# Performance work log

Hardware: AMD Instinct MI355X
Metric: run time of the kernel (lower is better)

Reference implementation:

```python
import jax, jax.numpy as jnp
import numpy as np

NEG_SLOPE = 0.2   # PyG GATConv default negative_slope
LN_EPS = 1e-5
SOFTMAX_EPS = 1e-16  # PyG softmax denominator eps


def setup_inputs() -> dict:
    key = jax.random.key(0)
    ks = jax.random.split(key, 6)
    N, IN, OUT, H, E = 100000, 128, 64, 2, 1600000
    X = jax.random.normal(ks[0], (N, IN), dtype=jnp.float32)
    edge_index = jax.random.randint(ks[1], (2, E), 0, N, dtype=jnp.int64)
    W = jax.random.normal(ks[2], (H * OUT, IN), dtype=jnp.float32) * 0.05
    att_src = jax.random.normal(ks[3], (H, OUT), dtype=jnp.float32) * 0.05
    att_dst = jax.random.normal(ks[4], (H, OUT), dtype=jnp.float32) * 0.05
    bias = jnp.zeros((OUT,), dtype=jnp.float32)
    ln_gamma = jnp.ones((OUT,), dtype=jnp.float32)
    ln_beta = jnp.zeros((OUT,), dtype=jnp.float32)
    return {"X": X, "edge_index": edge_index, "W": W, "att_src": att_src,
            "att_dst": att_dst, "bias": bias, "ln_gamma": ln_gamma, "ln_beta": ln_beta}


def reference(X, edge_index, W, att_src, att_dst, bias, ln_gamma, ln_beta):
    N = X.shape[0]
    H, F = att_src.shape
    # PyG GATConv default: add self-loops
    loops = jnp.arange(N, dtype=edge_index.dtype)
    src = jnp.concatenate([edge_index[0], loops])  # [Et]
    dst = jnp.concatenate([edge_index[1], loops])  # [Et]
    # linear projection: x' = X @ W^T  -> [N, H, F]
    x = (X @ W.T).reshape(N, H, F)
    # per-node attention logits  [N, H]
    a_src = jnp.einsum('nhf,hf->nh', x, att_src)
    a_dst = jnp.einsum('nhf,hf->nh', x, att_dst)
    # per-edge logits, leaky relu  [Et, H]
    e = jax.nn.leaky_relu(a_src[src] + a_dst[dst], NEG_SLOPE)
    # segment softmax over incoming edges of each dst node
    m = jax.ops.segment_max(e, dst, num_segments=N)          # [N, H]
    ex = jnp.exp(e - m[dst])
    denom = jax.ops.segment_sum(ex, dst, num_segments=N)     # [N, H]
    alpha = ex / (denom[dst] + SOFTMAX_EPS)                  # [Et, H]
    # weighted scatter-add of source features
    msg = x[src] * alpha[:, :, None]                         # [Et, H, F]
    out = jax.ops.segment_sum(msg, dst, num_segments=N)      # [N, H, F]
    # concat=False -> mean over heads, then bias
    out = out.mean(axis=1) + bias                            # [N, F]
    # LayerNorm over features
    mu = out.mean(axis=-1, keepdims=True)
    var = ((out - mu) ** 2).mean(axis=-1, keepdims=True)
    h = (out - mu) * jax.lax.rsqrt(var + LN_EPS) * ln_gamma + ln_beta
    return h
```

## Files before the change

kernel.cpp:

```cpp
#include <hip/hip_runtime.h>
#include <hip/hip_bf16.h>

#define NEG_SLOPE 0.2f
#define LN_EPS 1e-5f
#define SM_EPS 1e-16f

typedef __attribute__((ext_vector_type(8))) short bf16x8;
typedef __attribute__((ext_vector_type(4))) float f32x4;

__device__ inline unsigned short f2bf(float f) {
    unsigned u = __float_as_uint(f);
    return (unsigned short)((u + 0x7FFFu + ((u >> 16) & 1u)) >> 16);
}
__device__ inline float bf_lo(unsigned int v) { return __uint_as_float(v << 16); }
__device__ inline float bf_hi(unsigned int v) { return __uint_as_float(v & 0xffff0000u); }
__device__ inline float rdlane(float v, int l) {
    return __uint_as_float(__builtin_amdgcn_readlane(__float_as_uint(v), l));
}

#define NBIN 512
#define BCAP 4864
#define SCHUNK 4096
#define CURPAD 16

__global__ __launch_bounds__(256) void k_gemm(const float* __restrict__ X,
                                              const float* __restrict__ W,
                                              const float* __restrict__ att_src,
                                              const float* __restrict__ att_dst,
                                              unsigned int* __restrict__ xp,
                                              float2* __restrict__ aS,
                                              float2* __restrict__ aD,
                                              int* __restrict__ binCursor, int N) {
    __shared__ unsigned short Ws[128 * 136];
    __shared__ unsigned short Xs[64 * 136];
    const int t = threadIdx.x;
    const int b0 = blockIdx.x * 64;
    const int lane = t & 63;
    const int w = t >> 6;
    const int c15 = lane & 15;
    const int quad = lane >> 4;

    if (blockIdx.x == 0) {
        for (int i = t; i < NBIN; i += 256) binCursor[i * CURPAD] = i * BCAP;
    }

#pragma unroll
    for (int i = 0; i < 16; ++i) {
        int f = i * 256 + t;
        int nr = f >> 5;
        int q = f & 31;
        float4 v = reinterpret_cast<const float4*>(W)[nr * 32 + q];
        ushort4 b;
        b.x = f2bf(v.x); b.y = f2bf(v.y); b.z = f2bf(v.z); b.w = f2bf(v.w);
        *reinterpret_cast<ushort4*>(&Ws[nr * 136 + q * 4]) = b;
    }
#pragma unroll
    for (int i = 0; i < 8; ++i) {
        int f = i * 256 + t;
        int m = f >> 5;
        int q = f & 31;
        int gr = b0 + m;
        if (gr >= N) gr = N - 1;
        float4 v = reinterpret_cast<const float4*>(X)[(size_t)gr * 32 + q];
        ushort4 b;
        b.x = f2bf(v.x); b.y = f2bf(v.y); b.z = f2bf(v.z); b.w = f2bf(v.w);
        *reinterpret_cast<ushort4*>(&Xs[m * 136 + q * 4]) = b;
    }
    __syncthreads();

    f32x4 acc[8];
#pragma unroll
    for (int ct = 0; ct < 8; ++ct) acc[ct] = (f32x4){0.f, 0.f, 0.f, 0.f};

#pragma unroll
    for (int kc = 0; kc < 4; ++kc) {
        bf16x8 af = *reinterpret_cast<const bf16x8*>(
            &Xs[(w * 16 + c15) * 136 + kc * 32 + quad * 8]);
#pragma unroll
        for (int ct = 0; ct < 8; ++ct) {
            bf16x8 bfr = *reinterpret_cast<const bf16x8*>(
                &Ws[(ct * 16 + c15) * 136 + kc * 32 + quad * 8]);
            acc[ct] = __builtin_amdgcn_mfma_f32_16x16x32_bf16(af, bfr, acc[ct], 0, 0, 0);
        }
    }

    float attS[8], attD[8];
#pragma unroll
    for (int ct = 0; ct < 8; ++ct) {
        attS[ct] = att_src[ct * 16 + c15];
        attD[ct] = att_dst[ct * 16 + c15];
    }

#pragma unroll
    for (int r = 0; r < 4; ++r) {
        int row = b0 + w * 16 + quad * 4 + r;
        float s0 = 0.f, s1 = 0.f, d0 = 0.f, d1 = 0.f;
#pragma unroll
        for (int ct = 0; ct < 4; ++ct) {
            s0 += acc[ct][r] * attS[ct];
            d0 += acc[ct][r] * attD[ct];
            s1 += acc[ct + 4][r] * attS[ct + 4];
            d1 += acc[ct + 4][r] * attD[ct + 4];
        }
#pragma unroll
        for (int o = 1; o < 16; o <<= 1) {
            s0 += __shfl_xor(s0, o);
            s1 += __shfl_xor(s1, o);
            d0 += __shfl_xor(d0, o);
            d1 += __shfl_xor(d1, o);
        }
        if (row < N) {
#pragma unroll
            for (int ct = 0; ct < 4; ++ct) {
                unsigned int p = (unsigned int)f2bf(acc[ct][r]) |
                                 ((unsigned int)f2bf(acc[ct + 4][r]) << 16);
                xp[(size_t)row * 64 + ct * 16 + c15] = p;
            }
            if (c15 == 0) {
                aS[row] = make_float2(s0, s1);
                aD[row] = make_float2(d0, d1);
            }
        }
    }
}

__global__ __launch_bounds__(256) void k_scatter(const int* __restrict__ ei,
                                                 int* __restrict__ binCursor,
                                                 unsigned int* __restrict__ tmp,
                                                 int E) {
    __shared__ int off[NBIN];
    const int t = threadIdx.x;
    const int base = blockIdx.x * SCHUNK;

    int bn[16];
    unsigned int pe[16];
#pragma unroll
    for (int k = 0; k < 16; ++k) {
        int i = base + k * 256 + t;
        if (i < E) {
            int s = ei[i];
            int d = ei[E + i];
            bn[k] = d >> 8;
            pe[k] = ((unsigned)(d & 255) << 24) | (unsigned)s;
        } else {
            bn[k] = -1;
        }
    }

    for (int i = t; i < NBIN; i += 256) off[i] = 0;
    __syncthreads();
#pragma unroll
    for (int k = 0; k < 16; ++k)
        if (bn[k] >= 0) atomicAdd(&off[bn[k]], 1);
    __syncthreads();
    for (int i = t; i < NBIN; i += 256) {
        int h = off[i];
        off[i] = h ? atomicAdd(&binCursor[i * CURPAD], h) : 0;
    }
    __syncthreads();
#pragma unroll
    for (int k = 0; k < 16; ++k) {
        if (bn[k] >= 0) {
            int p = atomicAdd(&off[bn[k]], 1);
            tmp[p] = pe[k];
        }
    }
}

__global__ __launch_bounds__(512) void k_bucket(const unsigned int* __restrict__ tmp,
                                                const int* __restrict__ binCursor,
                                                unsigned int* __restrict__ csr,
                                                unsigned int* __restrict__ rowPtr,
                                                int N) {
    __shared__ int cnt[256];
    __shared__ int cur[256];
    __shared__ int lds[4];
    const int t = threadIdx.x;
    const int b = blockIdx.x;
    const int start = b * BCAP;
    int m = binCursor[b * CURPAD] - start;
    if (m > BCAP) m = BCAP;

    if (t < 256) cnt[t] = 0;
    __syncthreads();

    for (int k = t; k < m; k += 512) {
        atomicAdd(&cnt[tmp[start + k] >> 24], 1);
    }
    __syncthreads();

    const int lane = t & 63, w = t >> 6;
    int v = 0, incl = 0;
    if (t < 256) {
        v = cnt[t];
        incl = v;
#pragma unroll
        for (int o = 1; o < 64; o <<= 1) {
            int u = __shfl_up(incl, o);
            if (lane >= o) incl += u;
        }
        if (lane == 63) lds[w] = incl;
    }
    __syncthreads();
    if (t == 0) {
        int run = 0;
        for (int i = 0; i < 4; ++i) { int tv = lds[i]; lds[i] = run; run += tv; }
    }
    __syncthreads();
    if (t < 256) {
        int excl = lds[w] + incl - v;
        cur[t] = excl;
        int d = b * 256 + t;
        if (d < N) rowPtr[d] = (unsigned)(start + excl) | ((unsigned)v << 22);
    }
    __syncthreads();

    for (int k = t; k < m; k += 512) {
        unsigned int e = tmp[start + k];
        int p = atomicAdd(&cur[e >> 24], 1);
        csr[start + p] = e & 0x00FFFFFFu;
    }
}

__global__ __launch_bounds__(256) void k_agg(const unsigned int* __restrict__ xp,
                                             const float2* __restrict__ aS,
                                             const float2* __restrict__ aD,
                                             const unsigned int* __restrict__ rowPtr,
                                             const unsigned int* __restrict__ csr,
                                             const float* __restrict__ bias,
                                             const float* __restrict__ gamma,
                                             const float* __restrict__ beta,
                                             float* __restrict__ out, int N) {
    const int w = threadIdx.x >> 6, lane = threadIdx.x & 63;
    const int n = blockIdx.x * 4 + w;
    if (n >= N) return;

    const float* aSf = (const float*)aS;

    float2 a = aS[n];
    float2 ad2 = aD[n];
    float f0 = a.x + ad2.x; f0 = fmaxf(f0, NEG_SLOPE * f0);
    float f1 = a.y + ad2.y; f1 = fmaxf(f1, NEG_SLOPE * f1);
    float us0 = __expf(f0), us1 = __expf(f1);

    unsigned int vself = xp[((unsigned)n << 6) | lane];
    float S0 = us0 * bf_lo(vself);
    float S1 = us1 * bf_hi(vself);
    float D0 = us0, D1 = us1;

    unsigned int pr = rowPtr[n];
    const int jb = (int)(pr & 0x3FFFFFu);
    const int deg = (int)(pr >> 22);
    const int je = jb + deg;
    const int nb = (deg + 7) >> 3;

    const int eq = lane & 7;
    const int hsel = (lane >> 3) & 1;
    const float adv = hsel ? ad2.y : ad2.x;

    float Dacc = 0.f;
    int j = jb;
    unsigned int cc[8];
    unsigned int myc = 0;

    if (nb > 0) {
        int ju = __builtin_amdgcn_readfirstlane(jb);
        int last = __builtin_amdgcn_readfirstlane(je - 1);
#pragma unroll
        for (int q = 0; q < 8; ++q) {
            int idx = ju + q; if (idx > last) idx = last;
            cc[q] = csr[idx];
        }
        int mi = ju + eq; if (mi > last) mi = last;
        myc = csr[mi];
    }

    for (int bI = 0; bI < nb; ++bI) {
        const int limit = je - j;
        float av = aSf[(myc << 1) | (unsigned)hsel];
        unsigned int v[8];
#pragma unroll
        for (int q = 0; q < 8; ++q)
            v[q] = (xp + ((size_t)cc[q] << 6))[lane];
        unsigned int cn[8], mn;
        {
            int jn = (bI + 1 < nb) ? (j + 8) : jb;
            int ju = __builtin_amdgcn_readfirstlane(jn);
            int last = __builtin_amdgcn_readfirstlane(je - 1);
#pragma unroll
            for (int q = 0; q < 8; ++q) {
                int idx = ju + q; if (idx > last) idx = last;
                cn[q] = csr[idx];
            }
            int mi = ju + eq; if (mi > last) mi = last;
            mn = csr[mi];
        }
        float g = av + adv; g = fmaxf(g, NEG_SLOPE * g);
        float u = (eq < limit) ? __expf(g) : 0.f;
        Dacc += u;
#pragma unroll
        for (int q = 0; q < 8; ++q) {
            float u0 = rdlane(u, q);
            float u1 = rdlane(u, q + 8);
            S0 = fmaf(u0, bf_lo(v[q]), S0);
            S1 = fmaf(u1, bf_hi(v[q]), S1);
        }
#pragma unroll
        for (int q = 0; q < 8; ++q) cc[q] = cn[q];
        myc = mn;
        j += 8;
    }

    Dacc += __shfl_xor(Dacc, 1);
    Dacc += __shfl_xor(Dacc, 2);
    Dacc += __shfl_xor(Dacc, 4);
    D0 += rdlane(Dacc, 0);
    D1 += rdlane(Dacc, 8);

    float o = (0.5f / (D0 + SM_EPS)) * S0 + (0.5f / (D1 + SM_EPS)) * S1 + bias[lane];

    float mu = o;
#pragma unroll
    for (int d = 32; d > 0; d >>= 1) mu += __shfl_xor(mu, d);
    mu *= (1.0f / 64.0f);
    float dv = o - mu;
    float var = dv * dv;
#pragma unroll
    for (int d = 32; d > 0; d >>= 1) var += __shfl_xor(var, d);
    var *= (1.0f / 64.0f);
    out[(size_t)n * 64 + lane] = dv * rsqrtf(var + LN_EPS) * gamma[lane] + beta[lane];
}

extern "C" void kernel_launch(void* const* d_in, const int* in_sizes, int n_in,
                              void* d_out, int out_size, void* d_ws, size_t ws_size,
                              hipStream_t stream) {
    const float* X        = (const float*)d_in[0];
    const int*   ei       = (const int*)d_in[1];
    const float* W        = (const float*)d_in[2];
    const float* att_src  = (const float*)d_in[3];
    const float* att_dst  = (const float*)d_in[4];
    const float* bias     = (const float*)d_in[5];
    const float* ln_gamma = (const float*)d_in[6];
    const float* ln_beta  = (const float*)d_in[7];
    float* out = (float*)d_out;

    const int N = in_sizes[0] / 128;
    const int E = in_sizes[1] / 2;
    const int NBUCK = (N + 255) / 256;

    char* ws = (char*)d_ws;
    size_t off = 0;
    auto alloc = [&](size_t bytes) {
        size_t o = off;
        off += (bytes + 255) & ~(size_t)255;
        return o;
    };
    unsigned int* xp     = (unsigned int*)(ws + alloc((size_t)N * 64 * 4));
    float2* aS           = (float2*)(ws + alloc((size_t)N * 8));
    float2* aD           = (float2*)(ws + alloc((size_t)N * 8));
    unsigned int* rowPtr = (unsigned int*)(ws + alloc((size_t)N * 4));
    unsigned int* csr    = (unsigned int*)(ws + alloc((size_t)NBIN * BCAP * 4));
    unsigned int* tmp    = (unsigned int*)(ws + alloc((size_t)NBIN * BCAP * 4));
    int* binCursor       = (int*)(ws + alloc(NBIN * CURPAD * 4));

    k_gemm<<<(N + 63) / 64, 256, 0, stream>>>(X, W, att_src, att_dst, xp, aS, aD,
                                              binCursor, N);
    k_scatter<<<(E + SCHUNK - 1) / SCHUNK, 256, 0, stream>>>(ei, binCursor, tmp, E);
    k_bucket<<<NBUCK, 512, 0, stream>>>(tmp, binCursor, csr, rowPtr, N);
    k_agg<<<(N + 3) / 4, 256, 0, stream>>>(xp, aS, aD, rowPtr, csr,
                                           bias, ln_gamma, ln_beta, out, N);
}
```

Measured before the change: 221.5 us.

## Merge GEMM and edge scatter into one kernel to overlap independent work

Fuses the projection GEMM and the edge-binning scatter into a single launch, where the first SB blocks do the scatter and the rest do the GEMM, so the two independent stages can run at the same time on the GPU. The bin cursors become relative counts that start at zero, reset with a memset, and the bin base offset is added at use. This saves a kernel launch and lets the memory-bound scatter overlap with the compute-bound GEMM. The cost is an extra memset call and a shared-memory footprint sized for the larger GEMM branch, which may limit occupancy for the scatter blocks.

Measured after the change: 215.0 us. 3.0% less time.

```diff
diff --git a/kernel.cpp b/kernel.cpp
--- a/kernel.cpp
+++ b/kernel.cpp
@@ -23,26 +23,67 @@
 #define SCHUNK 4096
 #define CURPAD 16
 
-__global__ __launch_bounds__(256) void k_gemm(const float* __restrict__ X,
-                                              const float* __restrict__ W,
-                                              const float* __restrict__ att_src,
-                                              const float* __restrict__ att_dst,
-                                              unsigned int* __restrict__ xp,
-                                              float2* __restrict__ aS,
-                                              float2* __restrict__ aD,
-                                              int* __restrict__ binCursor, int N) {
-    __shared__ unsigned short Ws[128 * 136];
-    __shared__ unsigned short Xs[64 * 136];
+__global__ __launch_bounds__(256) void k_gs(const float* __restrict__ X,
+                                            const float* __restrict__ W,
+                                            const float* __restrict__ att_src,
+                                            const float* __restrict__ att_dst,
+                                            unsigned int* __restrict__ xp,
+                                            float2* __restrict__ aS,
+                                            float2* __restrict__ aD,
+                                            const int* __restrict__ ei,
+                                            int* __restrict__ binCursor,
+                                            unsigned int* __restrict__ tmp,
+                                            int N, int E, int SB) {
+    __shared__ __align__(16) char smem[52224];
     const int t = threadIdx.x;
-    const int b0 = blockIdx.x * 64;
+
+    if ((int)blockIdx.x < SB) {
+        int* off = (int*)smem;
+        const int base = blockIdx.x * SCHUNK;
+
+        int bn[16];
+        unsigned int pe[16];
+#pragma unroll
+        for (int k = 0; k < 16; ++k) {
+            int i = base + k * 256 + t;
+            if (i < E) {
+                int s = ei[i];
+                int d = ei[E + i];
+                bn[k] = d >> 8;
+                pe[k] = ((unsigned)(d & 255) << 24) | (unsigned)s;
+            } else {
+                bn[k] = -1;
+            }
+        }
+
+        for (int i = t; i < NBIN; i += 256) off[i] = 0;
+        __syncthreads();
+#pragma unroll
+        for (int k = 0; k < 16; ++k)
+            if (bn[k] >= 0) atomicAdd(&off[bn[k]], 1);
+        __syncthreads();
+        for (int i = t; i < NBIN; i += 256) {
+            int h = off[i];
+            off[i] = h ? (atomicAdd(&binCursor[i * CURPAD], h) + i * BCAP) : 0;
+        }
+        __syncthreads();
+#pragma unroll
+        for (int k = 0; k < 16; ++k) {
+            if (bn[k] >= 0) {
+                int p = atomicAdd(&off[bn[k]], 1);
+                tmp[p] = pe[k];
+            }
+        }
+        return;
+    }
+
+    unsigned short* Ws = (unsigned short*)smem;
+    unsigned short* Xs = (unsigned short*)(smem + 34816);
+    const int b0 = ((int)blockIdx.x - SB) * 64;
     const int lane = t & 63;
     const int w = t >> 6;
     const int c15 = lane & 15;
     const int quad = lane >> 4;
-
-    if (blockIdx.x == 0) {
-        for (int i = t; i < NBIN; i += 256) binCursor[i * CURPAD] = i * BCAP;
-    }
 
 #pragma unroll
     for (int i = 0; i < 16; ++i) {
@@ -120,49 +161,6 @@
                 aS[row] = make_float2(s0, s1);
                 aD[row] = make_float2(d0, d1);
             }
-        }
-    }
-}
-
-__global__ __launch_bounds__(256) void k_scatter(const int* __restrict__ ei,
-                                                 int* __restrict__ binCursor,
-                                                 unsigned int* __restrict__ tmp,
-                                                 int E) {
-    __shared__ int off[NBIN];
-    const int t = threadIdx.x;
-    const int base = blockIdx.x * SCHUNK;
-
-    int bn[16];
-    unsigned int pe[16];
-#pragma unroll
-    for (int k = 0; k < 16; ++k) {
-        int i = base + k * 256 + t;
-        if (i < E) {
-            int s = ei[i];
-            int d = ei[E + i];
-            bn[k] = d >> 8;
-            pe[k] = ((unsigned)(d & 255) << 24) | (unsigned)s;
-        } else {
-            bn[k] = -1;
-        }
-    }
-
-    for (int i = t; i < NBIN; i += 256) off[i] = 0;
-    __syncthreads();
-#pragma unroll
-    for (int k = 0; k < 16; ++k)
-        if (bn[k] >= 0) atomicAdd(&off[bn[k]], 1);
-    __syncthreads();
-    for (int i = t; i < NBIN; i += 256) {
-        int h = off[i];
-        off[i] = h ? atomicAdd(&binCursor[i * CURPAD], h) : 0;
-    }
-    __syncthreads();
-#pragma unroll
-    for (int k = 0; k < 16; ++k) {
-        if (bn[k] >= 0) {
-            int p = atomicAdd(&off[bn[k]], 1);
-            tmp[p] = pe[k];
         }
     }
 }
@@ -178,7 +176,7 @@
     const int t = threadIdx.x;
     const int b = blockIdx.x;
     const int start = b * BCAP;
-    int m = binCursor[b * CURPAD] - start;
+    int m = binCursor[b * CURPAD];
     if (m > BCAP) m = BCAP;
 
     if (t < 256) cnt[t] = 0;
@@ -347,6 +345,8 @@
     const int N = in_sizes[0] / 128;
     const int E = in_sizes[1] / 2;
     const int NBUCK = (N + 255) / 256;
+    const int SB = (E + SCHUNK - 1) / SCHUNK;
+    const int GB = (N + 63) / 64;
 
     char* ws = (char*)d_ws;
     size_t off = 0;
@@ -363,9 +363,9 @@
     unsigned int* tmp    = (unsigned int*)(ws + alloc((size_t)NBIN * BCAP * 4));
     int* binCursor       = (int*)(ws + alloc(NBIN * CURPAD * 4));
 
-    k_gemm<<<(N + 63) / 64, 256, 0, stream>>>(X, W, att_src, att_dst, xp, aS, aD,
-                                              binCursor, N);
-    k_scatter<<<(E + SCHUNK - 1) / SCHUNK, 256, 0, stream>>>(ei, binCursor, tmp, E);
+    hipMemsetAsync(binCursor, 0, (size_t)NBIN * CURPAD * 4, stream);
+    k_gs<<<SB + GB, 256, 0, stream>>>(X, W, att_src, att_dst, xp, aS, aD,
+                                      ei, binCursor, tmp, N, E, SB);
     k_bucket<<<NBUCK, 512, 0, stream>>>(tmp, binCursor, csr, rowPtr, N);
     k_agg<<<(N + 3) / 4, 256, 0, stream>>>(xp, aS, aD, rowPtr, csr,
                                            bias, ln_gamma, ln_beta, out, N);
```
